# Performance work log

Hardware: AMD Instinct MI355X
Metric: run time of the kernel (lower is better)

Reference implementation:

```python
import jax, jax.numpy as jnp
import numpy as np

B, S, DM, H, NM, PRED = 32, 512, 512, 8, 4, 96
DK = DM // H
C1 = (NM + 7) // 2  # 5
C2 = (NM + 7) // 4  # 2
FC_IN = C2 * (S // 2)  # 512
EPS_NORM = 1e-12
EPS_LN = 1e-5


def _pos_encoding(seq_len, d):
    pos = np.arange(seq_len, dtype=np.float32)[:, None]
    div = np.exp(np.arange(0, d, 2, dtype=np.float32) * (-np.log(10000.0) / d))
    pe = np.zeros((seq_len, d), np.float32)
    pe[:, 0::2] = np.sin(pos * div)
    pe[:, 1::2] = np.cos(pos * div)
    return jnp.asarray(pe)

PE = _pos_encoding(S, DM)


def setup_inputs() -> dict:
    key = jax.random.key(0)
    ks = jax.random.split(key, 24)
    g = lambda k, shape, s: (jax.random.normal(k, shape, dtype=jnp.float32) * s)
    inp = {
        "x": g(ks[0], (B, S, 7), 1.0),
        "emb_W": g(ks[1], (4, DM), 0.5),
        "emb_b": jnp.zeros((DM,), jnp.float32),
        "Wq": g(ks[2], (NM, DM, DM), DM ** -0.5),
        "bq": jnp.zeros((NM, DM), jnp.float32),
        "Wk": g(ks[3], (NM, DM, DM), DM ** -0.5),
        "bk": jnp.zeros((NM, DM), jnp.float32),
        "Wv": g(ks[4], (NM, DM, DM), DM ** -0.5),
        "bv": jnp.zeros((NM, DM), jnp.float32),
        "Wo": g(ks[5], (NM, DM, DM), DM ** -0.5),
        "bo": jnp.zeros((NM, DM), jnp.float32),
        "conv1_w": g(ks[6], (C1, NM * DM, 3), (NM * DM * 3) ** -0.5),
        "conv1_b": jnp.zeros((C1,), jnp.float32),
        "conv2_w": g(ks[7], (C2, C1, 3), (C1 * 3) ** -0.5),
        "conv2_b": jnp.zeros((C2,), jnp.float32),
        "fc1_w": g(ks[8], (FC_IN, 256), FC_IN ** -0.5),
        "fc1_b": jnp.zeros((256,), jnp.float32),
        "fc2_w": g(ks[9], (256, 128), 256 ** -0.5),
        "fc2_b": jnp.zeros((128,), jnp.float32),
        "fc3_w": g(ks[10], (128, PRED), 128 ** -0.5),
        "fc3_b": jnp.zeros((PRED,), jnp.float32),
        "ln_g": jnp.ones((PRED,), jnp.float32),
        "ln_b": jnp.zeros((PRED,), jnp.float32),
    }
    return inp


def _l2norm(v):
    n = jnp.linalg.norm(v, axis=-1, keepdims=True)
    return v / jnp.maximum(n, EPS_NORM)


def reference(x, emb_W, emb_b, Wq, bq, Wk, bk, Wv, bv, Wo, bo,
              conv1_w, conv1_b, conv2_w, conv2_b,
              fc1_w, fc1_b, fc2_w, fc2_b, fc3_w, fc3_b, ln_g, ln_b):
    b, s, _ = x.shape
    static = x[:, :, :3]                     # [B,S,3]
    dynamic = x[:, :, 3:]                    # [B,S,4]
    # per-modality input: [dynamic_i | static] -> [B,M,S,4]
    mod_in = jnp.concatenate([
        dynamic.transpose(0, 2, 1)[..., None],
        jnp.broadcast_to(static[:, None], (b, NM, s, 3)),
    ], axis=-1)
    h = jnp.einsum('bmsf,fd->bmsd', mod_in, emb_W) + emb_b  # shared embedding
    h = h + PE[None, None, :s, :]

    # per-modality multi-head cosine attention (stacked over modality axis m)
    def proj(W, bias):
        y = jnp.einsum('bmsd,mde->bmse', h, W) + bias[None, :, None, :]
        return y.reshape(b, NM, s, H, DK).transpose(0, 1, 3, 2, 4)  # [B,M,H,S,DK]

    Q = _l2norm(proj(Wq, bq))
    K = _l2norm(proj(Wk, bk))
    V = proj(Wv, bv)
    scores = jnp.einsum('bmhsk,bmhtk->bmhst', Q, K)
    attn = jax.nn.softmax(scores, axis=-1)
    ctx = jnp.einsum('bmhst,bmhtk->bmhsk', attn, V)
    ctx = ctx.transpose(0, 1, 3, 2, 4).reshape(b, NM, s, DM)
    out = jnp.einsum('bmsd,mde->bmse', ctx, Wo) + bo[None, :, None, :]

    # concat modalities along feature dim: [B,S,M*DM]
    combined = out.transpose(0, 2, 1, 3).reshape(b, s, NM * DM)

    # conv stack (NCW layout), kernel 3, padding 1
    c = combined.transpose(0, 2, 1)  # [B, M*DM, S]
    dn = ('NCH', 'OIH', 'NCH')
    c = jax.lax.conv_general_dilated(c, conv1_w, (1,), ((1, 1),), dimension_numbers=dn) + conv1_b[None, :, None]
    c = jax.nn.elu(c)
    c = jax.lax.conv_general_dilated(c, conv2_w, (1,), ((1, 1),), dimension_numbers=dn) + conv2_b[None, :, None]
    c = jax.nn.elu(c)
    # max pool k=2 stride=2
    c = c.reshape(b, C2, s // 2, 2).max(axis=-1)
    flat = c.reshape(b, -1)  # [B, FC_IN]

    z = jax.nn.elu(flat @ fc1_w + fc1_b)
    z = jax.nn.elu(z @ fc2_w + fc2_b)
    z = z @ fc3_w + fc3_b  # [B, PRED]

    mu = jnp.mean(z, axis=-1, keepdims=True)
    var = jnp.var(z, axis=-1, keepdims=True)
    z = (z - mu) / jnp.sqrt(var + EPS_LN) * ln_g + ln_b
    return z.reshape(b, PRED, 1)
```

## Files before the change

### kernel.cpp

```cpp
#include <hip/hip_runtime.h>
#include <math.h>

typedef unsigned short u16;
typedef unsigned int u32;
typedef __attribute__((ext_vector_type(8))) short short8;
typedef __attribute__((ext_vector_type(4))) float f32x4;
typedef __attribute__((ext_vector_type(16))) float f32x16;
typedef __attribute__((ext_vector_type(4))) u32 u32x4;
typedef __attribute__((ext_vector_type(2))) u32 u32x2;

__device__ inline u16 f2b(float f) {
  u32 u = __builtin_bit_cast(u32, f);
  u32 r = u + 0x7fffu + ((u >> 16) & 1u);
  return (u16)(r >> 16);
}
__device__ inline float b2f(u16 b) {
  return __builtin_bit_cast(float, (u32)b << 16);
}
__device__ inline u32 cvtpk(float lo, float hi) {
  u32 r;
  asm("v_cvt_pk_bf16_f32 %0, %1, %2" : "=v"(r) : "v"(lo), "v"(hi));
  return r;
}
__device__ inline float eluf(float x) { return x > 0.f ? x : expf(x) - 1.f; }

__device__ inline f32x4 mfma16(short8 a, short8 b, f32x4 c) {
  return __builtin_amdgcn_mfma_f32_16x16x32_bf16(a, b, c, 0, 0, 0);
}
__device__ inline f32x16 mfma32(short8 a, short8 b, f32x16 c) {
  return __builtin_amdgcn_mfma_f32_32x32x16_bf16(a, b, c, 0, 0, 0);
}
__device__ inline void gload16(const u16* g, u16* l) {
  __builtin_amdgcn_global_load_lds((__attribute__((address_space(1))) void*)(g),
                                   (__attribute__((address_space(3))) void*)(l),
                                   16, 0, 0);
}

__global__ __launch_bounds__(256) void prep_misc(
    const float* __restrict__ emb_b, const float* __restrict__ bq,
    const float* __restrict__ bk, const float* __restrict__ bv,
    const float* __restrict__ Wq, const float* __restrict__ Wk,
    const float* __restrict__ Wv, const float* __restrict__ embW,
    const float* __restrict__ Wo, const float* __restrict__ bo,
    const float* __restrict__ w1, u16* __restrict__ A_pe,
    float* __restrict__ pb_bias, float* __restrict__ EW,
    u16* __restrict__ WEFFT, float* __restrict__ bias_t,
    u16* __restrict__ WTqkv) {
  __shared__ float smem[64 * 65];
  const int bid = blockIdx.x, t = threadIdx.x;
  if (bid < 512) {
    int s = bid;
    float div = expf((2.f * t) * (-9.210340371976184f / 512.f));
    float arg = (float)s * div;
    A_pe[s * 512 + 2 * t] = f2b(sinf(arg) + emb_b[2 * t]);
    A_pe[s * 512 + 2 * t + 1] = f2b(cosf(arg) + emb_b[2 * t + 1]);
  } else if (bid < 536) {
    int i = (bid - 512) * 256 + t;
    int z = i >> 9, e = i & 511;
    int ty = z >> 2, m = z & 3;
    const float* bp = (ty == 0) ? bq : (ty == 1) ? bk : bv;
    pb_bias[i] = bp[m * 512 + e];
  } else if (bid < 584) {
    int idx = bid - 536;
    int z = idx >> 2, ch = idx & 3;
    const float* W =
        ((z < 4) ? Wq : (z < 8) ? Wk : Wv) + (long)(z & 3) * 262144;
    int el = t & 127, dh = t >> 7;
    int e = ch * 128 + el;
    float a[4] = {};
    for (int d = dh * 256; d < dh * 256 + 256; ++d) {
      float wv = W[(long)d * 512 + e];
#pragma unroll
      for (int f = 0; f < 4; ++f) a[f] += embW[f * 512 + d] * wv;
    }
#pragma unroll
    for (int f = 0; f < 4; ++f) smem[(dh * 4 + f) * 128 + el] = a[f];
    __syncthreads();
    if (t < 128) {
#pragma unroll
      for (int f = 0; f < 4; ++f)
        EW[((long)z * 4 + f) * 512 + e] =
            smem[f * 128 + el] + smem[(4 + f) * 128 + el];
    }
  } else if (bid < 1097) {
    const int wb = bid - 584;
    const int w = t >> 6, l = t & 63;
    if (wb < 512) {
      int idx = wb * 4 + w;
      int m = idx >> 9, d = idx & 511;
      const float* wrow = Wo + ((long)m * 512 + d) * 512;
      float a[15] = {};
#pragma unroll
      for (int i = 0; i < 8; ++i) {
        int e = l * 8 + i;
        float wv = wrow[e];
#pragma unroll
        for (int o = 0; o < 5; ++o)
#pragma unroll
          for (int k = 0; k < 3; ++k)
            a[o * 3 + k] += wv * w1[((long)o * 2048 + m * 512 + e) * 3 + k];
      }
#pragma unroll
      for (int j = 0; j < 15; ++j) {
        float v = a[j];
        for (int o = 1; o < 64; o <<= 1) v += __shfl_xor(v, o);
        if (l == 0) WEFFT[((long)m * 16 + j) * 512 + d] = f2b(v);
      }
      if (l == 0) WEFFT[((long)m * 16 + 15) * 512 + d] = 0;
    } else if (w == 0) {
      float a[15] = {};
      for (int c = l; c < 2048; c += 64) {
        float bv = bo[c];
#pragma unroll
        for (int o = 0; o < 5; ++o)
#pragma unroll
          for (int k = 0; k < 3; ++k)
            a[o * 3 + k] += bv * w1[((long)o * 2048 + c) * 3 + k];
      }
#pragma unroll
      for (int j = 0; j < 15; ++j) {
        float v = a[j];
        for (int o = 1; o < 64; o <<= 1) v += __shfl_xor(v, o);
        if (l == 0) bias_t[j] = v;
      }
      if (l == 0) bias_t[15] = 0.f;
    }
  } else {
    int bidt = bid - 1097;
    int mid = bidt >> 6, rest = bidt & 63;
    int d0 = (rest >> 3) * 64, e0 = (rest & 7) * 64;
    const float* W =
        ((mid < 4) ? Wq : (mid < 8) ? Wk : Wv) + (long)(mid & 3) * 262144;
    u16* WT = WTqkv + (long)mid * 262144;
    float(*tile)[65] = (float(*)[65])smem;
    int dr = t >> 2, ec = (t & 3) * 16;
#pragma unroll
    for (int j = 0; j < 16; j += 4) {
      float4 v = *(const float4*)&W[(long)(d0 + dr) * 512 + e0 + ec + j];
      tile[dr][ec + j] = v.x;
      tile[dr][ec + j + 1] = v.y;
      tile[dr][ec + j + 2] = v.z;
      tile[dr][ec + j + 3] = v.w;
    }
    __syncthreads();
    int er = t >> 2, dc = (t & 3) * 16;
    u16 tmp[16] __attribute__((aligned(16)));
#pragma unroll
    for (int j = 0; j < 16; ++j) tmp[j] = f2b(tile[dc + j][er]);
    *(short8*)&WT[(long)(e0 + er) * 512 + d0 + dc] = *(short8*)&tmp[0];
    *(short8*)&WT[(long)(e0 + er) * 512 + d0 + dc + 8] = *(short8*)&tmp[8];
  }
}

template <bool OBF>
__global__ __launch_bounds__(256) void gemm_bt(
    const u16* __restrict__ A, long sAz, int lda, const u16* __restrict__ BT,
    const float* __restrict__ bias, void* __restrict__ out, long sOz, int ldo) {
  __shared__ u16 As[128 * 32];
  __shared__ u16 Bs[128 * 32];
  const int z = blockIdx.z;
  const int tid = threadIdx.x, w = tid >> 6, l = tid & 63;
  const long row0 = (long)blockIdx.y * 128;
  const u16* Ab = A + (long)z * sAz + row0 * lda;
  const u16* Bb = BT + (long)z * 262144 + (long)blockIdx.x * 128 * 512;
  const u16* ga = Ab + (long)(w * 32 + (l >> 2)) * lda + (l & 3) * 8;
  const u16* gb = Bb + (long)(w * 32 + (l >> 2)) * 512 + (l & 3) * 8;
  u16* lA = As + w * 32 * 32;
  u16* lB = Bs + w * 32 * 32;
  f32x4 acc[4][4] = {};
  const int wr = (w >> 1) * 64, wc = (w & 1) * 64;
  for (int kt = 0; kt < 16; ++kt) {
    gload16(ga + kt * 32, lA);
    gload16(ga + kt * 32 + 16 * lda, lA + 16 * 32);
    gload16(gb + kt * 32, lB);
    gload16(gb + kt * 32 + 16 * 512, lB + 16 * 32);
    __syncthreads();
    short8 af[4], bf[4];
#pragma unroll
    for (int i = 0; i < 4; ++i)
      af[i] = *(const short8*)&As[(wr + i * 16 + (l & 15)) * 32 + (l >> 4) * 8];
#pragma unroll
    for (int i = 0; i < 4; ++i)
      bf[i] = *(const short8*)&Bs[(wc + i * 16 + (l & 15)) * 32 + (l >> 4) * 8];
#pragma unroll
    for (int i = 0; i < 4; ++i)
#pragma unroll
      for (int j = 0; j < 4; ++j) acc[i][j] = mfma16(af[i], bf[j], acc[i][j]);
    __syncthreads();
  }
  const int colB = blockIdx.x * 128 + wc;
#pragma unroll
  for (int i = 0; i < 4; ++i)
#pragma unroll
    for (int j = 0; j < 4; ++j) {
      int col = colB + j * 16 + (l & 15);
      float bb = bias[(long)z * 512 + col];
#pragma unroll
      for (int q = 0; q < 4; ++q) {
        long r = row0 + wr + i * 16 + (l >> 4) * 4 + q;
        float v = acc[i][j][q] + bb;
        if (OBF)
          ((u16*)out)[(long)z * sOz + r * ldo + col] = f2b(v);
        else
          ((float*)out)[(long)z * sOz + r * ldo + col] = v;
      }
    }
}

__global__ __launch_bounds__(256) void qkv_fused(
    const float* __restrict__ x, const float* __restrict__ EW,
    const u16* __restrict__ PB, u16* __restrict__ Q, u16* __restrict__ K,
    u16* __restrict__ VT, long mstride) {
  __shared__ float ews[3][4][64];
  __shared__ u16 vtile[64][72];
  const int bh = blockIdx.x;
  const int st = blockIdx.y;
  const int m = blockIdx.z;
  const int b = bh >> 3, h = bh & 7;
  const int hoff = h * 64;
  const int t = threadIdx.x;
  if (t < 192) {
    int ty = t >> 6, dk = t & 63;
#pragma unroll
    for (int f = 0; f < 4; ++f)
      ews[ty][f][dk] = EW[(((long)(ty * 4 + m)) * 4 + f) * 512 + hoff + dk];
  }
  __syncthreads();
  const int sr = t >> 2, cq = t & 3;
  const int s = st * 64 + sr;
  const long rid = (long)b * 512 + s;
  const float* xr = x + rid * 7;
  const float xd = xr[3 + m], x0 = xr[0], x1 = xr[1], x2 = xr[2];
  const long obase = (long)m * mstride + rid * 512 + hoff + cq * 16;

  float res[3][16];
#pragma unroll
  for (int ty = 0; ty < 3; ++ty) {
    const u16* pbp =
        PB + (((long)(ty * 4 + m)) * 512 + s) * 512 + hoff + cq * 16;
    short8 pbv0 = *(const short8*)pbp;
    short8 pbv1 = *(const short8*)(pbp + 8);
#pragma unroll
    for (int j = 0; j < 16; ++j) {
      int dk = cq * 16 + j;
      u16 pb = (u16)(j < 8 ? pbv0[j] : pbv1[j - 8]);
      res[ty][j] = xd * ews[ty][0][dk] + x0 * ews[ty][1][dk] +
                   x1 * ews[ty][2][dk] + x2 * ews[ty][3][dk] + b2f(pb);
    }
  }
#pragma unroll
  for (int ty = 0; ty < 2; ++ty) {
    float ss = 0.f;
#pragma unroll
    for (int j = 0; j < 16; ++j) ss += res[ty][j] * res[ty][j];
    ss += __shfl_xor(ss, 1);
    ss += __shfl_xor(ss, 2);
    float sc = 1.f / fmaxf(sqrtf(ss), 1e-12f);
    u32 o[8];
#pragma unroll
    for (int jj = 0; jj < 8; ++jj)
      o[jj] = cvtpk(res[ty][2 * jj] * sc, res[ty][2 * jj + 1] * sc);
    u16* P = ty ? K : Q;
    *(u32x4*)&P[obase] = *(u32x4*)&o[0];
    *(u32x4*)&P[obase + 8] = *(u32x4*)&o[4];
  }
  {
    u32 o[8];
#pragma unroll
    for (int jj = 0; jj < 8; ++jj)
      o[jj] = cvtpk(res[2][2 * jj], res[2][2 * jj + 1]);
    *(short8*)&vtile[sr][cq * 16] = *(short8*)&o[0];
    *(short8*)&vtile[sr][cq * 16 + 8] = *(short8*)&o[4];
  }
  __syncthreads();
  {
    int kr = t >> 2, sc2 = (t & 3) * 16;
    u16 tmp[16] __attribute__((aligned(16)));
#pragma unroll
    for (int j = 0; j < 16; ++j) tmp[j] = vtile[sc2 + j][kr];
    long gdst = (long)m * mstride + ((long)bh * 64 + kr) * 512 + st * 64 + sc2;
    *(short8*)&VT[gdst] = *(short8*)&tmp[0];
    *(short8*)&VT[gdst + 8] = *(short8*)&tmp[8];
  }
}

__global__ __launch_bounds__(512, 4) void attn_kernel(
    const u16* Qg, const u16* __restrict__ Kg, const u16* __restrict__ VTg,
    u16* ctxg, long mstride) {
  __shared__ u16 Kb[3][64][64];
  __shared__ u16 Vb[3][64][64];
  const int wgid = (blockIdx.x & 7) * 256 + (blockIdx.x >> 3);
  const int qp = wgid & 1;
  const int mz = wgid >> 1;
  const int m = mz & 3;
  const int bh = mz >> 2;
  const u16* Q = Qg + (long)m * mstride;
  const u16* K = Kg + (long)m * mstride;
  const u16* VT = VTg + (long)m * mstride;
  u16* ctx = ctxg + (long)m * mstride;
  const int b = bh >> 3, h = bh & 7;
  const int tid = threadIdx.x, w = tid >> 6, l = tid & 63;
  const int lq = l & 31, hi = l >> 5, l7 = l & 7;
  const long rowbase = (long)b * 512;
  const int hoff = h * 64;
  const int rw = l >> 3, gch = (l & 7) ^ rw;
  const int qrow = qp * 256 + w * 32;

  short8 qf[4];
  {
    const u16* qrp = Q + (rowbase + qrow + lq) * 512 + hoff + hi * 8;
#pragma unroll
    for (int dc = 0; dc < 4; ++dc) qf[dc] = *(const short8*)(qrp + dc * 16);
  }

  short8 ones;
#pragma unroll
  for (int i = 0; i < 8; ++i) ones[i] = (short)0x3F80;

  f32x16 o_acc[2] = {};
  f32x16 l_acc = {};

  const u16* Kgbase = K + rowbase * 512 + hoff + gch * 8;
  const u16* Vgbase = VT + (long)bh * 64 * 512 + gch * 8;

#define STAGE(bf, kt)                                                         \
  {                                                                           \
    int rr = w * 8;                                                           \
    gload16(Kgbase + (long)((kt)*64 + rr + rw) * 512, &Kb[bf][rr][0]);        \
    gload16(Vgbase + (long)(rr + rw) * 512 + (kt)*64, &Vb[bf][rr][0]);        \
  }

#define TILE(KT, CUR, NXT)                                                    \
  {                                                                           \
    if ((KT) < 7) {                                                           \
      STAGE(NXT, (KT) + 1);                                                   \
      asm volatile("s_waitcnt vmcnt(2)" ::: "memory");                        \
    } else {                                                                  \
      asm volatile("s_waitcnt vmcnt(0)" ::: "memory");                        \
    }                                                                         \
    __builtin_amdgcn_s_barrier();                                             \
    __builtin_amdgcn_sched_barrier(0);                                        \
    __builtin_amdgcn_s_setprio(1);                                            \
    _Pragma("unroll") for (int ktile = 0; ktile < 2; ++ktile) {               \
      f32x16 s = {};                                                          \
      _Pragma("unroll") for (int dc = 0; dc < 4; ++dc) {                      \
        short8 kf = *(const short8*)((const char*)&Kb[CUR][ktile * 32 + lq]   \
                                         [0] +                                \
                                     (((dc * 2 + hi) ^ l7) * 16));            \
        s = mfma32(kf, qf[dc], s);                                            \
      }                                                                       \
      float p[16];                                                            \
      _Pragma("unroll") for (int r = 0; r < 16; ++r) p[r] = __expf(s[r]);     \
      u32 s0a = cvtpk(p[0], p[1]), s0b = cvtpk(p[4], p[5]);                   \
      u32 s1a = cvtpk(p[2], p[3]), s1b = cvtpk(p[6], p[7]);                   \
      u32 s2a = cvtpk(p[8], p[9]), s2b = cvtpk(p[12], p[13]);                 \
      u32 s3a = cvtpk(p[10], p[11]), s3b = cvtpk(p[14], p[15]);               \
      asm("v_permlane32_swap_b32 %0, %1" : "+v"(s0a), "+v"(s0b));             \
      asm("v_permlane32_swap_b32 %0, %1" : "+v"(s1a), "+v"(s1b));             \
      asm("v_permlane32_swap_b32 %0, %1" : "+v"(s2a), "+v"(s2b));             \
      asm("v_permlane32_swap_b32 %0, %1" : "+v"(s3a), "+v"(s3b));             \
      u32x4 f0v = {s0a, s1a, s0b, s1b};                                       \
      u32x4 f1v = {s2a, s3a, s2b, s3b};                                       \
      short8 bf0 = __builtin_bit_cast(short8, f0v);                           \
      short8 bf1 = __builtin_bit_cast(short8, f1v);                           \
      _Pragma("unroll") for (int kk2 = 0; kk2 < 2; ++kk2) {                   \
        const int kc = ktile * 2 + kk2;                                       \
        short8 pb = kk2 ? bf1 : bf0;                                          \
        l_acc = mfma32(ones, pb, l_acc);                                      \
        _Pragma("unroll") for (int dt = 0; dt < 2; ++dt) {                    \
          short8 vf =                                                         \
              *(const short8*)((const char*)&Vb[CUR][dt * 32 + lq][0] +       \
                               (((kc * 2 + hi) ^ l7) * 16));                  \
          o_acc[dt] = mfma32(vf, pb, o_acc[dt]);                              \
        }                                                                     \
      }                                                                       \
    }                                                                         \
    __builtin_amdgcn_s_setprio(0);                                            \
    __builtin_amdgcn_sched_barrier(0);                                        \
  }

  STAGE(0, 0);
  TILE(0, 0, 1);
  TILE(1, 1, 2);
  TILE(2, 2, 0);
  TILE(3, 0, 1);
  TILE(4, 1, 2);
  TILE(5, 2, 0);
  TILE(6, 0, 1);
  TILE(7, 1, 2);
#undef TILE
#undef STAGE
  const float inv = 1.f / l_acc[0];
  u16* crow = ctx + (rowbase + qrow + lq) * 512 + hoff + hi * 4;
#pragma unroll
  for (int dt = 0; dt < 2; ++dt)
#pragma unroll
    for (int rq = 0; rq < 4; ++rq) {
      u32 w0 = cvtpk(o_acc[dt][rq * 4 + 0] * inv, o_acc[dt][rq * 4 + 1] * inv);
      u32 w1 = cvtpk(o_acc[dt][rq * 4 + 2] * inv, o_acc[dt][rq * 4 + 3] * inv);
      u32x2 pr = {w0, w1};
      *(u32x2*)&crow[dt * 32 + rq * 8] = pr;
    }
}

__global__ __launch_bounds__(64) void t_gemm(const u16* __restrict__ ctx4,
                                             const u16* __restrict__ WEFFT,
                                             float* __restrict__ t) {
  const int l = threadIdx.x;
  const long r0 = (long)blockIdx.x * 16;
  f32x4 acc = {};
#pragma unroll
  for (int m = 0; m < 4; ++m) {
    const u16* A =
        ctx4 + (long)m * 8388608 + (r0 + (l & 15)) * 512 + (l >> 4) * 8;
    const u16* Bb = WEFFT + m * 8192 + (l & 15) * 512 + (l >> 4) * 8;
#pragma unroll
    for (int kt = 0; kt < 16; ++kt) {
      short8 af = *(const short8*)(A + kt * 32);
      short8 bf = *(const short8*)(Bb + kt * 32);
      acc = mfma16(af, bf, acc);
    }
  }
#pragma unroll
  for (int q = 0; q < 4; ++q)
    t[(r0 + (l >> 4) * 4 + q) * 16 + (l & 15)] = acc[q];
}

__global__ __launch_bounds__(512) void tail_fused(
    const float* __restrict__ t, const float* __restrict__ bias_t,
    const float* __restrict__ b1, const float* __restrict__ w2,
    const float* __restrict__ b2, const float* __restrict__ fw1,
    const float* __restrict__ fb1, const float* __restrict__ fw2,
    const float* __restrict__ fb2, const float* __restrict__ fw3,
    const float* __restrict__ fb3, const float* __restrict__ g,
    const float* __restrict__ be, float* __restrict__ out) {
  __shared__ float ts[512][16];
  __shared__ float c1s[5][512];
  __shared__ float flat[512];
  __shared__ float z1p[2][256];
  __shared__ float z1[256];
  __shared__ float z2p[2][128];
  __shared__ float z2[128];
  __shared__ float z3[96];
  int b = blockIdx.x, tid = threadIdx.x;
  const float4* tsrc = (const float4*)(t + (long)b * 8192);
  float4* tdst = (float4*)&ts[0][0];
#pragma unroll
  for (int i = 0; i < 4; ++i) tdst[tid + i * 512] = tsrc[tid + i * 512];
  __syncthreads();
#pragma unroll
  for (int i = 0; i < 5; ++i) {
    int idx = tid + i * 512;
    int o = idx >> 9, s = idx & 511;
    float a = b1[o];
#pragma unroll
    for (int k = 0; k < 3; ++k) {
      int ss = s + k - 1;
      if (ss >= 0 && ss < 512) a += ts[ss][o * 3 + k] + bias_t[o * 3 + k];
    }
    c1s[o][s] = eluf(a);
  }
  __syncthreads();
  {
    int r = tid;
    int o = r >> 8, sp = r & 255;
    float mx = -1e30f;
#pragma unroll
    for (int sd = 0; sd < 2; ++sd) {
      int s = sp * 2 + sd;
      float a = b2[o];
#pragma unroll
      for (int ic = 0; ic < 5; ++ic)
#pragma unroll
        for (int k = 0; k < 3; ++k) {
          int ss = s + k - 1;
          if (ss >= 0 && ss < 512) a += c1s[ic][ss] * w2[(o * 5 + ic) * 3 + k];
        }
      mx = fmaxf(mx, eluf(a));
    }
    flat[r] = mx;
  }
  __syncthreads();
  {
    int o = tid & 255, part = tid >> 8;
    float a = 0.f;
    const float* wp = fw1 + (long)part * 256 * 256 + o;
    const float* xp = flat + part * 256;
#pragma unroll 8
    for (int i = 0; i < 256; ++i) a += xp[i] * wp[i * 256];
    z1p[part][o] = a;
  }
  __syncthreads();
  if (tid < 256) z1[tid] = eluf(fb1[tid] + z1p[0][tid] + z1p[1][tid]);
  __syncthreads();
  if (tid < 256) {
    int o = tid & 127, part = tid >> 7;
    float a = 0.f;
    const float* wp = fw2 + (long)part * 128 * 128 + o;
    const float* xp = z1 + part * 128;
#pragma unroll 8
    for (int i = 0; i < 128; ++i) a += xp[i] * wp[i * 128];
    z2p[part][o] = a;
  }
  __syncthreads();
  if (tid < 128) z2[tid] = eluf(fb2[tid] + z2p[0][tid] + z2p[1][tid]);
  __syncthreads();
  if (tid < 96) {
    float a = fb3[tid];
#pragma unroll 8
    for (int i = 0; i < 128; ++i) a += z2[i] * fw3[i * 96 + tid];
    z3[tid] = a;
  }
  __syncthreads();
  if (tid < 96) {
    float mu = 0.f;
    for (int j = 0; j < 96; ++j) mu += z3[j];
    mu *= (1.f / 96.f);
    float sq = 0.f;
    for (int j = 0; j < 96; ++j) {
      float d = z3[j] - mu;
      sq += d * d;
    }
    float var = sq * (1.f / 96.f);
    out[b * 96 + tid] = (z3[tid] - mu) / sqrtf(var + 1e-5f) * g[tid] + be[tid];
  }
}

extern "C" void kernel_launch(void* const* d_in, const int* in_sizes, int n_in,
                              void* d_out, int out_size, void* d_ws,
                              size_t ws_size, hipStream_t stream) {
  (void)in_sizes; (void)n_in; (void)out_size;
  const float* x    = (const float*)d_in[0];
  const float* embW = (const float*)d_in[1];
  const float* embB = (const float*)d_in[2];
  const float* Wq   = (const float*)d_in[3];
  const float* bq   = (const float*)d_in[4];
  const float* Wk   = (const float*)d_in[5];
  const float* bk   = (const float*)d_in[6];
  const float* Wv   = (const float*)d_in[7];
  const float* bv   = (const float*)d_in[8];
  const float* Wo   = (const float*)d_in[9];
  const float* bo   = (const float*)d_in[10];
  const float* c1w  = (const float*)d_in[11];
  const float* c1b  = (const float*)d_in[12];
  const float* c2w  = (const float*)d_in[13];
  const float* c2b  = (const float*)d_in[14];
  const float* f1w  = (const float*)d_in[15];
  const float* f1b  = (const float*)d_in[16];
  const float* f2w  = (const float*)d_in[17];
  const float* f2b_ = (const float*)d_in[18];
  const float* f3w  = (const float*)d_in[19];
  const float* f3b  = (const float*)d_in[20];
  const float* lng  = (const float*)d_in[21];
  const float* lnb  = (const float*)d_in[22];
  float* out = (float*)d_out;

  char* p = (char*)d_ws;
  const size_t NEED = 215736384;
  if (ws_size < NEED) return;
  const long MS = 8388608;

  u16*   A_pe    = (u16*)(p + 0);
  u16*   WTqkv   = (u16*)(p + 524288);
  float* pb_bias = (float*)(p + 6815744);
  float* EW      = (float*)(p + 6840320);
  u16*   PB      = (u16*)(p + 6938624);
  u16*   Q4      = (u16*)(p + 13230080);
  u16*   K4      = (u16*)(p + 80338944);
  u16*   VT4     = (u16*)(p + 147447808);
  u16*   ctx4    = Q4;
  u16*   WEFFT   = (u16*)(p + 214556672);
  float* bias_t  = (float*)(p + 214622208);
  float* t_buf   = (float*)(p + 214622272);

  prep_misc<<<1865, 256, 0, stream>>>(embB, bq, bk, bv, Wq, Wk, Wv, embW, Wo,
                                      bo, c1w, A_pe, pb_bias, EW, WEFFT,
                                      bias_t, WTqkv);
  gemm_bt<true><<<dim3(4, 4, 12), 256, 0, stream>>>(
      A_pe, 0, 512, WTqkv, pb_bias, (void*)PB, 262144, 512);

  qkv_fused<<<dim3(256, 8, 4), 256, 0, stream>>>(x, EW, PB, Q4, K4, VT4, MS);
  attn_kernel<<<2048, 512, 0, stream>>>(Q4, K4, VT4, ctx4, MS);

  t_gemm<<<1024, 64, 0, stream>>>(ctx4, WEFFT, t_buf);
  tail_fused<<<32, 512, 0, stream>>>(t_buf, bias_t, c1b, c2w, c2b, f1w, f1b,
                                     f2w, f2b_, f3w, f3b, lng, lnb, out);
}
```

Baseline: 225.7 us.

## Triple-buffer GEMM LDS loads and deepen attention K/V prefetch to two tiles

The projection GEMM now keeps three LDS buffers and issues the next k-tile's async loads before computing the current one, using a single barrier per step instead of two synchronous barriers. The attention kernel moves from three to four K/V buffers and prefetches two tiles ahead, lowering its occupancy hint from 4 to 2 blocks per SM. The goal is to hide global-load latency behind MFMA work. The cost is more LDS per block and possibly fewer resident blocks in the attention kernel.

```diff
diff --git a/kernel.cpp b/kernel.cpp
--- a/kernel.cpp
+++ b/kernel.cpp
@@ -156,8 +156,8 @@
 __global__ __launch_bounds__(256) void gemm_bt(
     const u16* __restrict__ A, long sAz, int lda, const u16* __restrict__ BT,
     const float* __restrict__ bias, void* __restrict__ out, long sOz, int ldo) {
-  __shared__ u16 As[128 * 32];
-  __shared__ u16 Bs[128 * 32];
+  __shared__ u16 As[3][128 * 32];
+  __shared__ u16 Bs[3][128 * 32];
   const int z = blockIdx.z;
   const int tid = threadIdx.x, w = tid >> 6, l = tid & 63;
   const long row0 = (long)blockIdx.y * 128;
@@ -165,29 +165,48 @@
   const u16* Bb = BT + (long)z * 262144 + (long)blockIdx.x * 128 * 512;
   const u16* ga = Ab + (long)(w * 32 + (l >> 2)) * lda + (l & 3) * 8;
   const u16* gb = Bb + (long)(w * 32 + (l >> 2)) * 512 + (l & 3) * 8;
-  u16* lA = As + w * 32 * 32;
-  u16* lB = Bs + w * 32 * 32;
   f32x4 acc[4][4] = {};
   const int wr = (w >> 1) * 64, wc = (w & 1) * 64;
-  for (int kt = 0; kt < 16; ++kt) {
-    gload16(ga + kt * 32, lA);
-    gload16(ga + kt * 32 + 16 * lda, lA + 16 * 32);
-    gload16(gb + kt * 32, lB);
-    gload16(gb + kt * 32 + 16 * 512, lB + 16 * 32);
-    __syncthreads();
-    short8 af[4], bf[4];
-#pragma unroll
-    for (int i = 0; i < 4; ++i)
-      af[i] = *(const short8*)&As[(wr + i * 16 + (l & 15)) * 32 + (l >> 4) * 8];
-#pragma unroll
-    for (int i = 0; i < 4; ++i)
-      bf[i] = *(const short8*)&Bs[(wc + i * 16 + (l & 15)) * 32 + (l >> 4) * 8];
-#pragma unroll
-    for (int i = 0; i < 4; ++i)
-#pragma unroll
-      for (int j = 0; j < 4; ++j) acc[i][j] = mfma16(af[i], bf[j], acc[i][j]);
-    __syncthreads();
-  }
+
+#define GSTAGE(BF, KT)                                                        \
+  {                                                                           \
+    gload16(ga + (KT)*32, &As[BF][w * 32 * 32]);                              \
+    gload16(ga + (KT)*32 + 16 * lda, &As[BF][w * 32 * 32 + 16 * 32]);         \
+    gload16(gb + (KT)*32, &Bs[BF][w * 32 * 32]);                              \
+    gload16(gb + (KT)*32 + 16 * 512, &Bs[BF][w * 32 * 32 + 16 * 32]);         \
+  }
+
+#define GTILE(KT, CUR, NXT)                                                   \
+  {                                                                           \
+    if ((KT) < 15) {                                                          \
+      GSTAGE(NXT, (KT) + 1);                                                  \
+      asm volatile("s_waitcnt vmcnt(4)" ::: "memory");                        \
+    } else {                                                                  \
+      asm volatile("s_waitcnt vmcnt(0)" ::: "memory");                        \
+    }                                                                         \
+    __builtin_amdgcn_s_barrier();                                             \
+    __builtin_amdgcn_sched_barrier(0);                                        \
+    short8 af[4], bf[4];                                                      \
+    _Pragma("unroll") for (int i = 0; i < 4; ++i) af[i] =                     \
+        *(const short8*)&As[CUR][(wr + i * 16 + (l & 15)) * 32 +              \
+                                 (l >> 4) * 8];                               \
+    _Pragma("unroll") for (int i = 0; i < 4; ++i) bf[i] =                     \
+        *(const short8*)&Bs[CUR][(wc + i * 16 + (l & 15)) * 32 +              \
+                                 (l >> 4) * 8];                               \
+    _Pragma("unroll") for (int i = 0; i < 4; ++i) _Pragma("unroll")           \
+        for (int j = 0; j < 4; ++j) acc[i][j] =                               \
+            mfma16(af[i], bf[j], acc[i][j]);                                  \
+    __builtin_amdgcn_sched_barrier(0);                                        \
+  }
+
+  GSTAGE(0, 0);
+  GTILE(0, 0, 1);  GTILE(1, 1, 2);  GTILE(2, 2, 0);  GTILE(3, 0, 1);
+  GTILE(4, 1, 2);  GTILE(5, 2, 0);  GTILE(6, 0, 1);  GTILE(7, 1, 2);
+  GTILE(8, 2, 0);  GTILE(9, 0, 1);  GTILE(10, 1, 2); GTILE(11, 2, 0);
+  GTILE(12, 0, 1); GTILE(13, 1, 2); GTILE(14, 2, 0); GTILE(15, 0, 1);
+#undef GTILE
+#undef GSTAGE
+
   const int colB = blockIdx.x * 128 + wc;
 #pragma unroll
   for (int i = 0; i < 4; ++i)
@@ -284,11 +303,11 @@
   }
 }
 
-__global__ __launch_bounds__(512, 4) void attn_kernel(
+__global__ __launch_bounds__(512, 2) void attn_kernel(
     const u16* Qg, const u16* __restrict__ Kg, const u16* __restrict__ VTg,
     u16* ctxg, long mstride) {
-  __shared__ u16 Kb[3][64][64];
-  __shared__ u16 Vb[3][64][64];
+  __shared__ u16 Kb[4][64][64];
+  __shared__ u16 Vb[4][64][64];
   const int wgid = (blockIdx.x & 7) * 256 + (blockIdx.x >> 3);
   const int qp = wgid & 1;
   const int mz = wgid >> 1;
@@ -332,8 +351,10 @@
 
 #define TILE(KT, CUR, NXT)                                                    \
   {                                                                           \
-    if ((KT) < 7) {                                                           \
-      STAGE(NXT, (KT) + 1);                                                   \
+    if ((KT) < 6) {                                                           \
+      STAGE(NXT, (KT) + 2);                                                   \
+      asm volatile("s_waitcnt vmcnt(4)" ::: "memory");                        \
+    } else if ((KT) == 6) {                                                   \
       asm volatile("s_waitcnt vmcnt(2)" ::: "memory");                        \
     } else {                                                                  \
       asm volatile("s_waitcnt vmcnt(0)" ::: "memory");                        \
@@ -380,14 +401,15 @@
   }
 
   STAGE(0, 0);
-  TILE(0, 0, 1);
-  TILE(1, 1, 2);
+  STAGE(1, 1);
+  TILE(0, 0, 2);
+  TILE(1, 1, 3);
   TILE(2, 2, 0);
-  TILE(3, 0, 1);
-  TILE(4, 1, 2);
-  TILE(5, 2, 0);
-  TILE(6, 0, 1);
-  TILE(7, 1, 2);
+  TILE(3, 3, 1);
+  TILE(4, 0, 2);
+  TILE(5, 1, 3);
+  TILE(6, 2, 0);
+  TILE(7, 3, 1);
 #undef TILE
 #undef STAGE
   const float inv = 1.f / l_acc[0];
```

Result: no change. 224.8 us (-0.4%).
